# Performance work log

Hardware: AMD Instinct MI355X
Metric: run time of the kernel (lower is better)

## Reference

```python
import jax, jax.numpy as jnp
import numpy as np
from jax import lax

B, MIN, DIN = 16, 8, 16
MOUT, DOUT = 8, 16
H, W = 32, 32
K, S, P, OP = 3, 2, 1, 1
NH, NW = 64, 64
ITERS = 2
EPS = 1e-7


def squash(s):
    # s: [..., D]; matches torch squash: factor * s / safe_norm
    sq = jnp.sum(s * s, axis=-1, keepdims=True)
    norm = jnp.sqrt(sq + EPS)
    return (sq / (1.0 + sq)) * s / norm


def setup_inputs() -> dict:
    key = jax.random.key(0)
    k1, k2, k3 = jax.random.split(key, 3)
    x = jax.random.normal(k1, (B, MIN, H, W, DIN), dtype=jnp.float32)
    # torch ConvTranspose2d weight layout: [in_ch, out_ch, kH, kW]
    w_deconv = jax.random.normal(k2, (MIN * DIN, MOUT * DOUT, K, K), dtype=jnp.float32) * 0.05
    b_deconv = jax.random.normal(k3, (MOUT * DOUT,), dtype=jnp.float32) * 0.05
    b_route = jnp.zeros((1, MOUT, NH, NW, MIN), dtype=jnp.float32)
    return {"x": x, "w_deconv": w_deconv, "b_deconv": b_deconv, "b_route": b_route}


def reference(x, w_deconv, b_deconv, b_route):
    Bb, Min, Hh, Ww, Din = x.shape
    # [B, Min, H, W, Din] -> [B, Min*Din, H, W]
    xc = jnp.transpose(x, (0, 1, 4, 2, 3)).reshape(Bb, Min * Din, Hh, Ww)
    # ConvTranspose2d == conv with lhs_dilation=stride and spatially-flipped, IO-swapped kernel
    wf = jnp.transpose(w_deconv, (1, 0, 2, 3))[:, :, ::-1, ::-1]  # [out, in, kH, kW]
    pad = (K - 1 - P, K - 1 - P + OP)
    y = lax.conv_general_dilated(
        xc, wf, window_strides=(1, 1), padding=[pad, pad],
        lhs_dilation=(S, S), dimension_numbers=("NCHW", "OIHW", "NCHW"))
    y = y + b_deconv[None, :, None, None]  # [B, Mout*Dout, NH, NW]
    nh, nw = y.shape[2], y.shape[3]
    # view([B, Mout, Dout, h, w, -1]).permute(0,1,3,4,5,2) -> [B, Mout, h, w, 1, Dout]
    pred = jnp.transpose(y.reshape(Bb, MOUT, DOUT, nh, nw, 1), (0, 1, 3, 4, 5, 2))
    # --- agreement routing ---
    c = jax.nn.softmax(b_route, axis=-1)                      # [1, Mout, h, w, Min]
    out = squash(jnp.sum(c[..., None] * pred, axis=-2))       # [B, Mout, h, w, Dout]
    b = b_route
    for _ in range(ITERS):
        b = b + jnp.sum(pred * out[..., None, :], axis=-1)    # [B, Mout, h, w, Min]
        c = jax.nn.softmax(b, axis=-1)
        out = squash(jnp.sum(pred * c[..., None], axis=-2))
    return out
```

## Files before the change

kernel.cpp:

```cpp
#include <hip/hip_runtime.h>
#include <hip/hip_bf16.h>
#include <math.h>


typedef __attribute__((ext_vector_type(8))) __bf16 bf16x8;
typedef __attribute__((ext_vector_type(4))) float f32x4;

#define XBF_ELEMS (16 * 8 * 32 * 32 * 16)

__global__ __launch_bounds__(256) void prep(const float* __restrict__ x,
                                            const float* __restrict__ w,
                                            __hip_bfloat16* __restrict__ xbf,
                                            __hip_bfloat16* __restrict__ wl) {
    const int bx = blockIdx.x;
    if (bx < 1024) {
        const int i = (bx * 256 + threadIdx.x) * 8;
        float4 a = *(const float4*)(x + i);
        float4 b = *(const float4*)(x + i + 4);
        union { bf16x8 v; __hip_bfloat162 h[4]; } u;
        u.h[0] = __float22bfloat162_rn(make_float2(a.x, a.y));
        u.h[1] = __float22bfloat162_rn(make_float2(a.z, a.w));
        u.h[2] = __float22bfloat162_rn(make_float2(b.x, b.y));
        u.h[3] = __float22bfloat162_rn(make_float2(b.z, b.w));
        *(bf16x8*)(xbf + i) = u.v;
    } else {
        const int idx = (bx - 1024) * 256 + threadIdx.x;
        const int ci  = idx / 1152;
        const int rem = idx - ci * 1152;
        const int co  = rem / 9;
        const int tap = rem - co * 9;
        const int s = ci >> 5, quad = (ci >> 3) & 3, j = ci & 7;
        const int t = co >> 4, n16 = co & 15;
        const int dst = ((((tap * 4 + s) * 8 + t) * 64) + quad * 16 + n16) * 8 + j;
        wl[dst] = __float2bfloat16(w[idx]);
    }
}

template <int PH, int PW>
__device__ __forceinline__ void caps_body(
    const __hip_bfloat16* __restrict__ xbf, const __hip_bfloat16* __restrict__ wl,
    const float* __restrict__ bias, float* __restrict__ out, int nh)
{
    const int tid = threadIdx.x, lane = tid & 63, wv = tid >> 6;
    const int q = blockIdx.y, b = blockIdx.z;
    const int rp = wv >> 1, ch = wv & 1;
    const int rw0 = q * 4 + rp * 2;
    const int n16  = lane & 15;
    const int quad = lane >> 4;
    const int c    = ch * 16 + n16;

    float bb[4];
    #pragma unroll
    for (int tt = 0; tt < 4; ++tt) bb[tt] = bias[(nh * 4 + tt) * 16 + n16];

    const __hip_bfloat16* xq = xbf + b * 131072 + (quad >> 1) * 16384 + (quad & 1) * 8;
    const __hip_bfloat16* wq = wl + lane * 8 + (nh * 4) * 512;

    f32x4 acc[2][4];
    #pragma unroll
    for (int r = 0; r < 2; ++r)
        #pragma unroll
        for (int tt = 0; tt < 4; ++tt) acc[r][tt] = (f32x4){0.f, 0.f, 0.f, 0.f};

    #pragma unroll
    for (int khi = 0; khi < (PH ? 2 : 1); ++khi) {
        const int kh = PH ? khi * 2 : 1;
        const int dh = PH ? (1 - khi) : 0;
        const int ih0 = rw0 + dh, ih1 = ih0 + 1;
        const bool v0 = (ih0 < 32), v1 = (ih1 < 32);
        const int ih0c = v0 ? ih0 : 31, ih1c = v1 ? ih1 : 31;
        #pragma unroll
        for (int kwi = 0; kwi < (PW ? 2 : 1); ++kwi) {
            const int kw = PW ? kwi * 2 : 1;
            const int dw = PW ? (1 - kwi) : 0;
            const int iw = c + dw;
            const bool vw = (iw < 32);
            const int iwc = vw ? iw : 31;
            const int tap = kh * 3 + kw;
            const __hip_bfloat16* a0p = xq + ih0c * 512 + iwc * 16;
            const __hip_bfloat16* a1p = xq + ih1c * 512 + iwc * 16;
            const __hip_bfloat16* wb  = wq + tap * 16384;
            #pragma unroll
            for (int s = 0; s < 4; ++s) {
                bf16x8 a0 = *(const bf16x8*)(a0p + s * 32768);
                bf16x8 a1 = *(const bf16x8*)(a1p + s * 32768);
                if (!(v0 && vw)) a0 = (bf16x8){};
                if (!(v1 && vw)) a1 = (bf16x8){};
                #pragma unroll
                for (int tt = 0; tt < 4; ++tt) {
                    bf16x8 bf = *(const bf16x8*)(wb + (s * 8 + tt) * 512);
                    acc[0][tt] = __builtin_amdgcn_mfma_f32_16x16x32_bf16(a0, bf, acc[0][tt], 0, 0, 0);
                    acc[1][tt] = __builtin_amdgcn_mfma_f32_16x16x32_bf16(a1, bf, acc[1][tt], 0, 0, 0);
                }
            }
        }
    }

    #pragma unroll
    for (int row = 0; row < 2; ++row) {
        const int oh = (rw0 + row) * 2 + PH;
        float y[4][4], sq[4][4];
        #pragma unroll
        for (int tt = 0; tt < 4; ++tt)
            #pragma unroll
            for (int r = 0; r < 4; ++r) {
                y[tt][r]  = acc[row][tt][r] + bb[tt];
                sq[tt][r] = y[tt][r] * y[tt][r];
            }
        #pragma unroll
        for (int st = 1; st <= 8; st <<= 1)
            #pragma unroll
            for (int tt = 0; tt < 4; ++tt)
                #pragma unroll
                for (int r = 0; r < 4; ++r)
                    sq[tt][r] += __shfl_xor(sq[tt][r], st, 64);
        #pragma unroll
        for (int tt = 0; tt < 4; ++tt)
            #pragma unroll
            for (int r = 0; r < 4; ++r) {
                const float s2 = sq[tt][r];
                const float f  = s2 / ((1.f + s2) * sqrtf(s2 + 1e-7f));
                const int ow = (ch * 16 + quad * 4 + r) * 2 + PW;
                __builtin_nontemporal_store(
                    y[tt][r] * f,
                    out + (((b * 8 + nh * 4 + tt) * 64 + oh) * 64 + ow) * 16 + n16);
            }
    }
}

__global__ __launch_bounds__(256, 4) void caps_mfma(
    const __hip_bfloat16* __restrict__ xbf, const __hip_bfloat16* __restrict__ wl,
    const float* __restrict__ bias, float* __restrict__ out)
{
    const int nh = blockIdx.x >> 2;
    switch (blockIdx.x & 3) {
    case 0:  caps_body<0, 0>(xbf, wl, bias, out, nh); break;
    case 1:  caps_body<0, 1>(xbf, wl, bias, out, nh); break;
    case 2:  caps_body<1, 0>(xbf, wl, bias, out, nh); break;
    default: caps_body<1, 1>(xbf, wl, bias, out, nh); break;
    }
}

extern "C" void kernel_launch(void* const* d_in, const int* in_sizes, int n_in,
                              void* d_out, int out_size, void* d_ws, size_t ws_size,
                              hipStream_t stream) {
    const float* x    = (const float*)d_in[0];
    const float* wgt  = (const float*)d_in[1];
    const float* bias = (const float*)d_in[2];
    float* out = (float*)d_out;

    __hip_bfloat16* xbf = (__hip_bfloat16*)d_ws;
    __hip_bfloat16* wlb = xbf + XBF_ELEMS;

    prep<<<1024 + 576, 256, 0, stream>>>(x, wgt, xbf, wlb);
    caps_mfma<<<dim3(8, 8, 16), 256, 0, stream>>>(xbf, wlb, bias, out);
}
```

Measured before the change: 94.66 us.

## Stage weights in LDS and balance work across parity classes

Each block now copies the weight slice it needs (32 KB of bf16) into shared memory before the MFMA loop and reads B fragments from LDS rather than global memory. Work is split so every block does about the same MFMA count: the single-tap parity class takes all 8 capsule types, the two-tap classes take 4, and the four-tap class takes 2, which raises the grid from 8 to 9 blocks in x. This targets load imbalance between parity classes and repeated global weight loads. The cost is a 32 KB LDS allocation per block, which may limit occupancy, plus an added barrier.

```diff
diff --git a/kernel.cpp b/kernel.cpp
--- a/kernel.cpp
+++ b/kernel.cpp
@@ -36,50 +36,65 @@
     }
 }
 
-template <int PH, int PW>
+template <int PH, int PW, int NT>
 __device__ __forceinline__ void caps_body(
     const __hip_bfloat16* __restrict__ xbf, const __hip_bfloat16* __restrict__ wl,
-    const float* __restrict__ bias, float* __restrict__ out, int nh)
+    const float* __restrict__ bias, float* __restrict__ out,
+    __hip_bfloat16* bsh, int t0)
 {
+    constexpr int NH = PH ? 2 : 1, NW = PW ? 2 : 1;
+    constexpr int CHE = NT * 512;
     const int tid = threadIdx.x, lane = tid & 63, wv = tid >> 6;
     const int q = blockIdx.y, b = blockIdx.z;
-    const int rp = wv >> 1, ch = wv & 1;
+
+    #pragma unroll
+    for (int it = 0; it < 8; ++it) {
+        const int idx    = it * 2048 + tid * 8;
+        const int c2     = idx / CHE;
+        const int within = idx % CHE;
+        const int s  = c2 & 3, ti = c2 >> 2;
+        const int kh = PH ? (ti / NW) * 2 : 1;
+        const int kw = PW ? (ti % NW) * 2 : 1;
+        const int tap = kh * 3 + kw;
+        *(bf16x8*)(bsh + idx) =
+            *(const bf16x8*)(wl + ((tap * 4 + s) * 8 + t0) * 512 + within);
+    }
+    __syncthreads();
+
+    const int rp = wv >> 1, chf = wv & 1;
     const int rw0 = q * 4 + rp * 2;
     const int n16  = lane & 15;
     const int quad = lane >> 4;
-    const int c    = ch * 16 + n16;
+    const int c    = chf * 16 + n16;
 
-    float bb[4];
+    float bb[NT];
     #pragma unroll
-    for (int tt = 0; tt < 4; ++tt) bb[tt] = bias[(nh * 4 + tt) * 16 + n16];
+    for (int tt = 0; tt < NT; ++tt) bb[tt] = bias[(t0 + tt) * 16 + n16];
 
     const __hip_bfloat16* xq = xbf + b * 131072 + (quad >> 1) * 16384 + (quad & 1) * 8;
-    const __hip_bfloat16* wq = wl + lane * 8 + (nh * 4) * 512;
 
-    f32x4 acc[2][4];
+    f32x4 acc[2][NT];
     #pragma unroll
     for (int r = 0; r < 2; ++r)
         #pragma unroll
-        for (int tt = 0; tt < 4; ++tt) acc[r][tt] = (f32x4){0.f, 0.f, 0.f, 0.f};
+        for (int tt = 0; tt < NT; ++tt) acc[r][tt] = (f32x4){0.f, 0.f, 0.f, 0.f};
 
     #pragma unroll
-    for (int khi = 0; khi < (PH ? 2 : 1); ++khi) {
-        const int kh = PH ? khi * 2 : 1;
+    for (int khi = 0; khi < NH; ++khi) {
         const int dh = PH ? (1 - khi) : 0;
         const int ih0 = rw0 + dh, ih1 = ih0 + 1;
         const bool v0 = (ih0 < 32), v1 = (ih1 < 32);
         const int ih0c = v0 ? ih0 : 31, ih1c = v1 ? ih1 : 31;
         #pragma unroll
-        for (int kwi = 0; kwi < (PW ? 2 : 1); ++kwi) {
-            const int kw = PW ? kwi * 2 : 1;
+        for (int kwi = 0; kwi < NW; ++kwi) {
             const int dw = PW ? (1 - kwi) : 0;
             const int iw = c + dw;
             const bool vw = (iw < 32);
             const int iwc = vw ? iw : 31;
-            const int tap = kh * 3 + kw;
+            const int ti = khi * NW + kwi;
             const __hip_bfloat16* a0p = xq + ih0c * 512 + iwc * 16;
             const __hip_bfloat16* a1p = xq + ih1c * 512 + iwc * 16;
-            const __hip_bfloat16* wb  = wq + tap * 16384;
+            const __hip_bfloat16* wb  = bsh + ti * (4 * CHE) + lane * 8;
             #pragma unroll
             for (int s = 0; s < 4; ++s) {
                 bf16x8 a0 = *(const bf16x8*)(a0p + s * 32768);
@@ -87,8 +102,8 @@
                 if (!(v0 && vw)) a0 = (bf16x8){};
                 if (!(v1 && vw)) a1 = (bf16x8){};
                 #pragma unroll
-                for (int tt = 0; tt < 4; ++tt) {
-                    bf16x8 bf = *(const bf16x8*)(wb + (s * 8 + tt) * 512);
+                for (int tt = 0; tt < NT; ++tt) {
+                    bf16x8 bf = *(const bf16x8*)(wb + s * CHE + tt * 512);
                     acc[0][tt] = __builtin_amdgcn_mfma_f32_16x16x32_bf16(a0, bf, acc[0][tt], 0, 0, 0);
                     acc[1][tt] = __builtin_amdgcn_mfma_f32_16x16x32_bf16(a1, bf, acc[1][tt], 0, 0, 0);
                 }
@@ -99,9 +114,9 @@
     #pragma unroll
     for (int row = 0; row < 2; ++row) {
         const int oh = (rw0 + row) * 2 + PH;
-        float y[4][4], sq[4][4];
+        float y[NT][4], sq[NT][4];
         #pragma unroll
-        for (int tt = 0; tt < 4; ++tt)
+        for (int tt = 0; tt < NT; ++tt)
             #pragma unroll
             for (int r = 0; r < 4; ++r) {
                 y[tt][r]  = acc[row][tt][r] + bb[tt];
@@ -110,20 +125,20 @@
         #pragma unroll
         for (int st = 1; st <= 8; st <<= 1)
             #pragma unroll
-            for (int tt = 0; tt < 4; ++tt)
+            for (int tt = 0; tt < NT; ++tt)
                 #pragma unroll
                 for (int r = 0; r < 4; ++r)
                     sq[tt][r] += __shfl_xor(sq[tt][r], st, 64);
         #pragma unroll
-        for (int tt = 0; tt < 4; ++tt)
+        for (int tt = 0; tt < NT; ++tt)
             #pragma unroll
             for (int r = 0; r < 4; ++r) {
                 const float s2 = sq[tt][r];
                 const float f  = s2 / ((1.f + s2) * sqrtf(s2 + 1e-7f));
-                const int ow = (ch * 16 + quad * 4 + r) * 2 + PW;
+                const int ow = (chf * 16 + quad * 4 + r) * 2 + PW;
                 __builtin_nontemporal_store(
                     y[tt][r] * f,
-                    out + (((b * 8 + nh * 4 + tt) * 64 + oh) * 64 + ow) * 16 + n16);
+                    out + (((b * 8 + t0 + tt) * 64 + oh) * 64 + ow) * 16 + n16);
             }
     }
 }
@@ -132,13 +147,12 @@
     const __hip_bfloat16* __restrict__ xbf, const __hip_bfloat16* __restrict__ wl,
     const float* __restrict__ bias, float* __restrict__ out)
 {
-    const int nh = blockIdx.x >> 2;
-    switch (blockIdx.x & 3) {
-    case 0:  caps_body<0, 0>(xbf, wl, bias, out, nh); break;
-    case 1:  caps_body<0, 1>(xbf, wl, bias, out, nh); break;
-    case 2:  caps_body<1, 0>(xbf, wl, bias, out, nh); break;
-    default: caps_body<1, 1>(xbf, wl, bias, out, nh); break;
-    }
+    __shared__ __hip_bfloat16 bsh[16384];
+    const int bx = blockIdx.x;
+    if      (bx == 0) caps_body<0, 0, 8>(xbf, wl, bias, out, bsh, 0);
+    else if (bx <  3) caps_body<0, 1, 4>(xbf, wl, bias, out, bsh, (bx - 1) * 4);
+    else if (bx <  5) caps_body<1, 0, 4>(xbf, wl, bias, out, bsh, (bx - 3) * 4);
+    else              caps_body<1, 1, 2>(xbf, wl, bias, out, bsh, (bx - 5) * 2);
 }
 
 extern "C" void kernel_launch(void* const* d_in, const int* in_sizes, int n_in,
@@ -153,5 +167,5 @@
     __hip_bfloat16* wlb = xbf + XBF_ELEMS;
 
     prep<<<1024 + 576, 256, 0, stream>>>(x, wgt, xbf, wlb);
-    caps_mfma<<<dim3(8, 8, 16), 256, 0, stream>>>(xbf, wlb, bias, out);
+    caps_mfma<<<dim3(9, 8, 16), 256, 0, stream>>>(xbf, wlb, bias, out);
 }
```

Result: no change. 96.44 us (+1.9%).
